# Performance work log

Measured on AMD Instinct MI355X. Metric: run time of the kernel, lower is better.

The kernel has to match this reference:

```python
import jax, jax.numpy as jnp
import numpy as np

B, T, D, U = 32, 2048, 1024, 1024

def setup_inputs() -> dict:
    key = jax.random.key(0)
    ks = jax.random.split(key, 6)
    scale = 1.0 / np.sqrt(D)
    return {
        "features": jax.random.normal(ks[0], (B, T, D), dtype=jnp.float32),
        "hidden": jax.random.normal(ks[1], (B, D), dtype=jnp.float32),
        "W1": jax.random.normal(ks[2], (D, U), dtype=jnp.float32) * scale,
        "b1": jnp.zeros((U,), dtype=jnp.float32),
        "W2": jax.random.normal(ks[3], (D, U), dtype=jnp.float32) * scale,
        "b2": jnp.zeros((U,), dtype=jnp.float32),
        "V": jax.random.normal(ks[4], (U, 1), dtype=jnp.float32) * (1.0 / np.sqrt(U)),
        "bV": jnp.zeros((1,), dtype=jnp.float32),
    }

def reference(features, hidden, W1, b1, W2, b2, V, bV):
    # features: [B,T,D], hidden: [B,D]
    proj_f = jnp.einsum('btd,du->btu', features, W1) + b1          # [B,T,U]
    proj_h = (hidden @ W2 + b2)[:, None, :]                        # [B,1,U]
    score = jnp.tanh(proj_f + proj_h)                              # [B,T,U]
    logits = jnp.einsum('btu,uo->bto', score, V) + bV              # [B,T,1]
    attention_weights = jax.nn.softmax(logits, axis=1)             # [B,T,1]
    context_vector = jnp.sum(attention_weights * features, axis=1) # [B,D]
    return context_vector, attention_weights
```

## Files before the change

kernel.cpp:

```cpp
#include <hip/hip_runtime.h>
#include <hip/hip_bf16.h>
#include <hip/hip_fp16.h>

#define B_ 32
#define T_ 2048
#define D_ 1024
#define U_ 1024
#define M_ (B_ * T_)
#define NT_ 16

typedef _Float16 f16x8 __attribute__((ext_vector_type(8)));
typedef float f32x4 __attribute__((ext_vector_type(4)));

__device__ __forceinline__ float fast_tanh(float x) {
    float xc = fminf(fmaxf(x, -10.f), 10.f);
    float e = __expf(2.f * xc);
    return 1.f - 2.f / (e + 1.f);
}

__device__ __forceinline__ void load_lds16(const void* g, void* l) {
    __builtin_amdgcn_global_load_lds(
        (const __attribute__((address_space(1))) void*)g,
        (__attribute__((address_space(3))) void*)l, 16, 0, 0);
}

__global__ void precastT_kernel(const float* __restrict__ in,
                                _Float16* __restrict__ out) {
    int mt = blockIdx.x;
    int t = threadIdx.x;
    int slot = t & 15, kb0 = t >> 4;
    const float* src = in + ((size_t)mt * 16 + slot) * D_;
    _Float16* dst = out + (size_t)mt * 16384 + slot * 8;
    #pragma unroll
    for (int i = 0; i < 8; ++i) {
        int kb = kb0 + i * 16;
        f32x4 a = *(const f32x4*)(src + kb * 8);
        f32x4 b = *(const f32x4*)(src + kb * 8 + 4);
        f16x8 h;
        h[0] = (_Float16)a[0]; h[1] = (_Float16)a[1];
        h[2] = (_Float16)a[2]; h[3] = (_Float16)a[3];
        h[4] = (_Float16)b[0]; h[5] = (_Float16)b[1];
        h[6] = (_Float16)b[2]; h[7] = (_Float16)b[3];
        *(f16x8*)(dst + kb * 128) = h;
    }
}

__global__ void transpose_cast_W1T_kernel(const float* __restrict__ W1,
                                          _Float16* __restrict__ W1T) {
    int u = blockIdx.x * 256 + threadIdx.x;
    int d0 = blockIdx.y * 64;
    _Float16* dst = W1T + (size_t)(u >> 4) * 16384 + (u & 15) * 8;
    for (int j8 = 0; j8 < 8; ++j8) {
        f16x8 h;
        #pragma unroll
        for (int j = 0; j < 8; ++j)
            h[j] = (_Float16)W1[(size_t)(d0 + j8 * 8 + j) * U_ + u];
        *(f16x8*)(dst + (size_t)(d0 / 8 + j8) * 128) = h;
    }
}

__global__ void proj_h_partial_kernel(const float* __restrict__ hidden,
                                      const float* __restrict__ W2,
                                      float* __restrict__ pph) {
    int u = blockIdx.x * 256 + threadIdx.x;
    int c = blockIdx.y;
    __shared__ float hb[32][128];
    for (int i = threadIdx.x; i < 32 * 128; i += 256)
        hb[i >> 7][i & 127] = hidden[(i >> 7) * D_ + c * 128 + (i & 127)];
    __syncthreads();
    float acc[32] = {};
    for (int d = 0; d < 128; ++d) {
        float w = W2[(size_t)(c * 128 + d) * U_ + u];
        #pragma unroll
        for (int b = 0; b < 32; ++b) acc[b] = fmaf(hb[b][d], w, acc[b]);
    }
    #pragma unroll
    for (int b = 0; b < 32; ++b)
        pph[((size_t)c * 32 + b) * U_ + u] = acc[b];
}

__global__ void proj_h_combine_kernel(const float* __restrict__ pph,
                                      const float* __restrict__ b1,
                                      const float* __restrict__ b2,
                                      float* __restrict__ ph) {
    int u = blockIdx.x * 256 + threadIdx.x;
    float bias = b1[u] + b2[u];
    for (int b = 0; b < 32; ++b) {
        float s = bias;
        #pragma unroll
        for (int c = 0; c < 8; ++c) s += pph[((size_t)c * 32 + b) * U_ + u];
        ph[b * U_ + u] = s;
    }
}


#define LOAD_AF(dst, mtb, s) do { \
    const char* a_ = fT + ((size_t)(mtb) << 15) + (s) * 1024 + l16; \
    _Pragma("unroll") \
    for (int m_ = 0; m_ < 8; ++m_) \
        dst[m_] = *(const f16x8*)(a_ + (m_ << 15)); \
} while (0)

#define READ_BF(s) do { \
    _Pragma("unroll") \
    for (int n_ = 0; n_ < 4; ++n_) \
        bfc[n_] = *(const f16x8*)(lB + n_ * 32768 + (s) * 1024 + l16); \
} while (0)

#define MFMA_STEP(AF) do { \
    __builtin_amdgcn_s_setprio(1); \
    _Pragma("unroll") \
    for (int m_ = 0; m_ < 8; ++m_) \
        _Pragma("unroll") \
        for (int n_ = 0; n_ < 4; ++n_) \
            acc[m_][n_] = __builtin_amdgcn_mfma_f32_16x16x32_f16( \
                AF[m_], bfc[n_], acc[m_][n_], 0, 0, 0); \
    __builtin_amdgcn_s_setprio(0); \
} while (0)

__global__ __launch_bounds__(512, 2)
void gemm_logits_v7_kernel(const _Float16* __restrict__ featT,
                           const _Float16* __restrict__ W1T,
                           const float* __restrict__ ph,
                           const float* __restrict__ V,
                           float* __restrict__ part)
{
    __shared__ __align__(16) _Float16 Bs[65536];

    int bid = blockIdx.x;
    int xcd = bid & 7, local = bid >> 3;
    int mtcg = xcd * 2 + (local >> 4);
    int nt = local & 15;

    int tid = threadIdx.x;
    int l = tid & 63, w = tid >> 6;
    int l16 = l * 16;
    const char* fT = (const char*)featT;
    const char* lB = (const char*)Bs;

    {
        const char* src = (const char*)W1T + (size_t)nt * 131072;
        #pragma unroll
        for (int i = 0; i < 16; ++i)
            load_lds16(src + i * 8192 + tid * 16, (char*)Bs + i * 8192 + tid * 16);
    }

    f16x8 afA[8], afB[8], bfc[4];
    f32x4 acc[8][4] = {};

    LOAD_AF(afA, mtcg * 256 + w * 8, 0);

    float Vv[4];
    #pragma unroll
    for (int n = 0; n < 4; ++n) Vv[n] = V[nt * 64 + n * 16 + (l & 15)];

    asm volatile("s_waitcnt vmcnt(0)" ::: "memory");
    __builtin_amdgcn_s_barrier();

    #pragma unroll 1
    for (int c = 0; c < 4; ++c) {
        int mtb = mtcg * 256 + c * 64 + w * 8;
        int mtbn = (c < 3) ? (mtb + 64) : mtb;

        #pragma unroll 1
        for (int s = 0; s < 32; s += 2) {
            READ_BF(s);
            LOAD_AF(afB, mtb, s + 1);
            MFMA_STEP(afA);
            READ_BF(s + 1);
            if (s < 30) LOAD_AF(afA, mtb, s + 2);
            else        LOAD_AF(afA, mtbn, 0);
            MFMA_STEP(afB);
        }

        int row0 = mtcg * 4096 + c * 1024 + w * 128;
        const float* phb = ph + (row0 >> 11) * U_;
        float phv[4];
        #pragma unroll
        for (int n = 0; n < 4; ++n) phv[n] = phb[nt * 64 + n * 16 + (l & 15)];
        #pragma unroll
        for (int m = 0; m < 8; ++m) {
            #pragma unroll
            for (int r = 0; r < 4; ++r) {
                float p = 0.f;
                #pragma unroll
                for (int n = 0; n < 4; ++n)
                    p = fmaf(fast_tanh(acc[m][n][r] + phv[n]), Vv[n], p);
                p += __shfl_xor(p, 1, 64);
                p += __shfl_xor(p, 2, 64);
                p += __shfl_xor(p, 4, 64);
                p += __shfl_xor(p, 8, 64);
                if ((l & 15) == 0)
                    part[(size_t)nt * M_ + row0 + m * 16 + (l >> 4) * 4 + r] = p;
            }
        }
        #pragma unroll
        for (int m = 0; m < 8; ++m)
            #pragma unroll
            for (int n = 0; n < 4; ++n)
                acc[m][n] = (f32x4){0.f, 0.f, 0.f, 0.f};
    }
}

__global__ void softmax_kernel(const float* __restrict__ part,
                               float* __restrict__ wout) {
    int b = blockIdx.x;
    int tid = threadIdx.x;
    __shared__ float red[8];
    float lg[8];
    #pragma unroll
    for (int j = 0; j < 8; ++j) {
        int t = tid + j * 256;
        float s = 0.f;
        #pragma unroll
        for (int p = 0; p < NT_; ++p)
            s += part[(size_t)p * M_ + b * T_ + t];
        lg[j] = s;
    }
    float mx = lg[0];
    #pragma unroll
    for (int j = 1; j < 8; ++j) mx = fmaxf(mx, lg[j]);
    #pragma unroll
    for (int off = 1; off < 64; off <<= 1) mx = fmaxf(mx, __shfl_xor(mx, off, 64));
    int wv = tid >> 6;
    if ((tid & 63) == 0) red[wv] = mx;
    __syncthreads();
    mx = fmaxf(fmaxf(red[0], red[1]), fmaxf(red[2], red[3]));
    float e[8];
    float sum = 0.f;
    #pragma unroll
    for (int j = 0; j < 8; ++j) { e[j] = __expf(lg[j] - mx); sum += e[j]; }
    #pragma unroll
    for (int off = 1; off < 64; off <<= 1) sum += __shfl_xor(sum, off, 64);
    if ((tid & 63) == 0) red[4 + wv] = sum;
    __syncthreads();
    sum = red[4] + red[5] + red[6] + red[7];
    float inv = 1.f / sum;
    #pragma unroll
    for (int j = 0; j < 8; ++j)
        wout[b * T_ + tid + j * 256] = e[j] * inv;
}

__global__ void context_v7_kernel(const _Float16* __restrict__ featT,
                                  const float* __restrict__ w,
                                  float* __restrict__ ctx) {
    int b = blockIdx.x;
    int dc = blockIdx.y;
    int t = threadIdx.x;
    __shared__ float wLds[2048];
    for (int i = t; i < 2048; i += 256) wLds[i] = w[b * T_ + i];
    __syncthreads();

    float acc[8] = {};
    const char* base = (const char*)featT + (size_t)b * 128 * 32768 + dc * 4096 + t * 16;
    int slot = t & 15;
    #pragma unroll 4
    for (int mt = 0; mt < 128; ++mt) {
        f16x8 v = *(const f16x8*)(base + (size_t)mt * 32768);
        float wt = wLds[mt * 16 + slot];
        #pragma unroll
        for (int j = 0; j < 8; ++j) acc[j] = fmaf(wt, (float)v[j], acc[j]);
    }
    #pragma unroll
    for (int j = 0; j < 8; ++j) {
        acc[j] += __shfl_xor(acc[j], 1, 64);
        acc[j] += __shfl_xor(acc[j], 2, 64);
        acc[j] += __shfl_xor(acc[j], 4, 64);
        acc[j] += __shfl_xor(acc[j], 8, 64);
    }
    if ((t & 15) == 0) {
        float* o = ctx + b * D_ + dc * 128 + (t >> 4) * 8;
        #pragma unroll
        for (int j = 0; j < 8; ++j) o[j] = acc[j];
    }
}

extern "C" void kernel_launch(void* const* d_in, const int* in_sizes, int n_in,
                              void* d_out, int out_size, void* d_ws, size_t ws_size,
                              hipStream_t stream) {
    const float* features = (const float*)d_in[0];
    const float* hidden   = (const float*)d_in[1];
    const float* W1       = (const float*)d_in[2];
    const float* b1       = (const float*)d_in[3];
    const float* W2       = (const float*)d_in[4];
    const float* b2       = (const float*)d_in[5];
    const float* V        = (const float*)d_in[6];

    float* ctx_out = (float*)d_out;
    float* w_out   = ctx_out + B_ * D_;

    char* ws = (char*)d_ws;
    _Float16* W1T  = (_Float16*)ws;
    float* ph      = (float*)(ws + (size_t)(2 << 20));
    float* pph     = (float*)(ws + (size_t)(2 << 20) + (1 << 17));
    float* part    = (float*)(ws + (size_t)(4 << 20));
    _Float16* featT = (_Float16*)(ws + (size_t)(8 << 20));

    transpose_cast_W1T_kernel<<<dim3(4, 16), 256, 0, stream>>>(W1, W1T);
    proj_h_partial_kernel<<<dim3(4, 8), 256, 0, stream>>>(hidden, W2, pph);
    proj_h_combine_kernel<<<4, 256, 0, stream>>>(pph, b1, b2, ph);
    precastT_kernel<<<4096, 256, 0, stream>>>(features, featT);

    gemm_logits_v7_kernel<<<256, 512, 0, stream>>>(featT, W1T, ph, V, part);

    softmax_kernel<<<B_, 256, 0, stream>>>(part, w_out);
    context_v7_kernel<<<dim3(B_, 8), 256, 0, stream>>>(featT, w_out, ctx_out);
}
```

Measured before the change: 324.5 us.

## Split GEMM into smaller per-block tiles and stage precast through swizzled LDS

```diff
diff --git a/kernel.cpp b/kernel.cpp
--- a/kernel.cpp
+++ b/kernel.cpp
@@ -26,21 +26,34 @@
 
 __global__ void precastT_kernel(const float* __restrict__ in,
                                 _Float16* __restrict__ out) {
+    __shared__ __align__(16) _Float16 lds[16 * 1024];
     int mt = blockIdx.x;
     int t = threadIdx.x;
-    int slot = t & 15, kb0 = t >> 4;
-    const float* src = in + ((size_t)mt * 16 + slot) * D_;
+    const float* src = in + (size_t)mt * 16384;
+    #pragma unroll
+    for (int i = 0; i < 4; ++i) {
+        int o = (i * 256 + t) * 16;
+        int r = o >> 10, c = o & 1023;
+        f32x4 a0 = *(const f32x4*)(src + o);
+        f32x4 a1 = *(const f32x4*)(src + o + 4);
+        f32x4 a2 = *(const f32x4*)(src + o + 8);
+        f32x4 a3 = *(const f32x4*)(src + o + 12);
+        f16x8 h0, h1;
+        h0[0]=(_Float16)a0[0]; h0[1]=(_Float16)a0[1]; h0[2]=(_Float16)a0[2]; h0[3]=(_Float16)a0[3];
+        h0[4]=(_Float16)a1[0]; h0[5]=(_Float16)a1[1]; h0[6]=(_Float16)a1[2]; h0[7]=(_Float16)a1[3];
+        h1[0]=(_Float16)a2[0]; h1[1]=(_Float16)a2[1]; h1[2]=(_Float16)a2[2]; h1[3]=(_Float16)a2[3];
+        h1[4]=(_Float16)a3[0]; h1[5]=(_Float16)a3[1]; h1[6]=(_Float16)a3[2]; h1[7]=(_Float16)a3[3];
+        int u0 = c >> 3, swz = r & 7;
+        *(f16x8*)((char*)lds + r * 2048 + ((u0 ^ swz) << 4)) = h0;
+        *(f16x8*)((char*)lds + r * 2048 + (((u0 + 1) ^ swz) << 4)) = h1;
+    }
+    __syncthreads();
+    int slot = t & 15, kb0 = t >> 4, ssw = slot & 7;
     _Float16* dst = out + (size_t)mt * 16384 + slot * 8;
     #pragma unroll
     for (int i = 0; i < 8; ++i) {
         int kb = kb0 + i * 16;
-        f32x4 a = *(const f32x4*)(src + kb * 8);
-        f32x4 b = *(const f32x4*)(src + kb * 8 + 4);
-        f16x8 h;
-        h[0] = (_Float16)a[0]; h[1] = (_Float16)a[1];
-        h[2] = (_Float16)a[2]; h[3] = (_Float16)a[3];
-        h[4] = (_Float16)b[0]; h[5] = (_Float16)b[1];
-        h[6] = (_Float16)b[2]; h[7] = (_Float16)b[3];
+        f16x8 h = *(const f16x8*)((char*)lds + slot * 2048 + ((kb ^ ssw) << 4));
         *(f16x8*)(dst + kb * 128) = h;
     }
 }
@@ -94,10 +107,10 @@
 }
 
 
-#define LOAD_AF(dst, mtb, s) do { \
-    const char* a_ = fT + ((size_t)(mtb) << 15) + (s) * 1024 + l16; \
+#define LOAD_AF(dst, s) do { \
+    const char* a_ = aT + (s) * 1024; \
     _Pragma("unroll") \
-    for (int m_ = 0; m_ < 8; ++m_) \
+    for (int m_ = 0; m_ < 4; ++m_) \
         dst[m_] = *(const f16x8*)(a_ + (m_ << 15)); \
 } while (0)
 
@@ -110,7 +123,7 @@
 #define MFMA_STEP(AF) do { \
     __builtin_amdgcn_s_setprio(1); \
     _Pragma("unroll") \
-    for (int m_ = 0; m_ < 8; ++m_) \
+    for (int m_ = 0; m_ < 4; ++m_) \
         _Pragma("unroll") \
         for (int n_ = 0; n_ < 4; ++n_) \
             acc[m_][n_] = __builtin_amdgcn_mfma_f32_16x16x32_f16( \
@@ -118,8 +131,8 @@
     __builtin_amdgcn_s_setprio(0); \
 } while (0)
 
-__global__ __launch_bounds__(512, 2)
-void gemm_logits_v7_kernel(const _Float16* __restrict__ featT,
+__global__ __launch_bounds__(1024, 4)
+void gemm_logits_v8_kernel(const _Float16* __restrict__ featT,
                            const _Float16* __restrict__ W1T,
                            const float* __restrict__ ph,
                            const float* __restrict__ V,
@@ -129,26 +142,27 @@
 
     int bid = blockIdx.x;
     int xcd = bid & 7, local = bid >> 3;
-    int mtcg = xcd * 2 + (local >> 4);
     int nt = local & 15;
+    int mg = xcd * 8 + (local >> 4);
 
     int tid = threadIdx.x;
     int l = tid & 63, w = tid >> 6;
     int l16 = l * 16;
-    const char* fT = (const char*)featT;
     const char* lB = (const char*)Bs;
+
+    const char* aT = (const char*)featT + ((size_t)(mg * 64 + w * 4) << 15) + l16;
 
     {
         const char* src = (const char*)W1T + (size_t)nt * 131072;
         #pragma unroll
-        for (int i = 0; i < 16; ++i)
-            load_lds16(src + i * 8192 + tid * 16, (char*)Bs + i * 8192 + tid * 16);
-    }
-
-    f16x8 afA[8], afB[8], bfc[4];
-    f32x4 acc[8][4] = {};
-
-    LOAD_AF(afA, mtcg * 256 + w * 8, 0);
+        for (int i = 0; i < 8; ++i)
+            load_lds16(src + i * 16384 + tid * 16, (char*)Bs + i * 16384 + tid * 16);
+    }
+
+    f16x8 afA[4], afB[4], bfc[4];
+    f32x4 acc[4][4] = {};
+
+    LOAD_AF(afA, 0);
 
     float Vv[4];
     #pragma unroll
@@ -158,47 +172,35 @@
     __builtin_amdgcn_s_barrier();
 
     #pragma unroll 1
-    for (int c = 0; c < 4; ++c) {
-        int mtb = mtcg * 256 + c * 64 + w * 8;
-        int mtbn = (c < 3) ? (mtb + 64) : mtb;
-
-        #pragma unroll 1
-        for (int s = 0; s < 32; s += 2) {
-            READ_BF(s);
-            LOAD_AF(afB, mtb, s + 1);
-            MFMA_STEP(afA);
-            READ_BF(s + 1);
-            if (s < 30) LOAD_AF(afA, mtb, s + 2);
-            else        LOAD_AF(afA, mtbn, 0);
-            MFMA_STEP(afB);
-        }
-
-        int row0 = mtcg * 4096 + c * 1024 + w * 128;
-        const float* phb = ph + (row0 >> 11) * U_;
-        float phv[4];
-        #pragma unroll
-        for (int n = 0; n < 4; ++n) phv[n] = phb[nt * 64 + n * 16 + (l & 15)];
-        #pragma unroll
-        for (int m = 0; m < 8; ++m) {
-            #pragma unroll
-            for (int r = 0; r < 4; ++r) {
-                float p = 0.f;
-                #pragma unroll
-                for (int n = 0; n < 4; ++n)
-                    p = fmaf(fast_tanh(acc[m][n][r] + phv[n]), Vv[n], p);
-                p += __shfl_xor(p, 1, 64);
-                p += __shfl_xor(p, 2, 64);
-                p += __shfl_xor(p, 4, 64);
-                p += __shfl_xor(p, 8, 64);
-                if ((l & 15) == 0)
-                    part[(size_t)nt * M_ + row0 + m * 16 + (l >> 4) * 4 + r] = p;
-            }
-        }
-        #pragma unroll
-        for (int m = 0; m < 8; ++m)
+    for (int s = 0; s < 32; s += 2) {
+        READ_BF(s);
+        LOAD_AF(afB, s + 1);
+        MFMA_STEP(afA);
+        READ_BF(s + 1);
+        if (s < 30) LOAD_AF(afA, s + 2);
+        MFMA_STEP(afB);
+    }
+
+    int row0 = mg * 1024 + w * 64;
+    const float* phb = ph + (mg >> 1) * U_;
+    float phv[4];
+    #pragma unroll
+    for (int n = 0; n < 4; ++n) phv[n] = phb[nt * 64 + n * 16 + (l & 15)];
+    #pragma unroll
+    for (int m = 0; m < 4; ++m) {
+        #pragma unroll
+        for (int r = 0; r < 4; ++r) {
+            float p = 0.f;
             #pragma unroll
             for (int n = 0; n < 4; ++n)
-                acc[m][n] = (f32x4){0.f, 0.f, 0.f, 0.f};
+                p = fmaf(fast_tanh(acc[m][n][r] + phv[n]), Vv[n], p);
+            p += __shfl_xor(p, 1, 64);
+            p += __shfl_xor(p, 2, 64);
+            p += __shfl_xor(p, 4, 64);
+            p += __shfl_xor(p, 8, 64);
+            if ((l & 15) == 0)
+                part[(size_t)nt * M_ + row0 + m * 16 + (l >> 4) * 4 + r] = p;
+        }
     }
 }
 
@@ -301,7 +303,7 @@
     proj_h_combine_kernel<<<4, 256, 0, stream>>>(pph, b1, b2, ph);
     precastT_kernel<<<4096, 256, 0, stream>>>(features, featT);
 
-    gemm_logits_v7_kernel<<<256, 512, 0, stream>>>(featT, W1T, ph, V, part);
+    gemm_logits_v8_kernel<<<1024, 1024, 0, stream>>>(featT, W1T, ph, V, part);
 
     softmax_kernel<<<B_, 256, 0, stream>>>(part, w_out);
     context_v7_kernel<<<dim3(B_, 8), 256, 0, stream>>>(featT, w_out, ctx_out);
```

Measured after the change: 314.8 us. -3.0%, faster.
